# Kernel optimization log

Measured on AMD Instinct MI355X. Metric: run time of the kernel, lower is better.

## Reference

```python
import jax, jax.numpy as jnp
import numpy as np

OH, OW = 32, 32          # adaptive pool output size
NUM_KERNELS = 2
LATENT = 100             # latent_dims = [100, 100]
S = (OH // 2) * (OW // 2)  # in_spatial = 256


def adaptive_avg_pool(x, oh, ow):
    # exact-divisor adaptive avg pool == block mean
    B, C, H, W = x.shape
    return x.reshape(B, C, oh, H // oh, ow, W // ow).mean(axis=(3, 5))


def setup_inputs() -> dict:
    key = jax.random.key(0)
    k1, k2, k3, k4 = jax.random.split(key, 4)
    x = jax.random.normal(k1, (8, 512, 128, 128), dtype=jnp.float32)
    scale = 1.0 / np.sqrt(S)
    psi_w = jax.random.normal(k2, (NUM_KERNELS, S, LATENT), dtype=jnp.float32) * scale  # visible->latent proj
    phi_w = jax.random.normal(k3, (NUM_KERNELS, S, LATENT), dtype=jnp.float32) * scale  # latent->visible proj
    out_w = jax.random.normal(k4, (S, S), dtype=jnp.float32) * scale                    # output linear over spatial feats
    return {"x": x, "psi_w": psi_w, "phi_w": phi_w, "out_w": out_w}


def reference(x, psi_w, phi_w, out_w):
    B, C, H, W = x.shape
    # GAP: adaptive average pool to (OH, OW)
    xg = adaptive_avg_pool(x, OH, OW)                                   # [B,C,32,32]
    # internal 2x2 avg pool (accounts for in_spatial = h/2 * ceil(w/2))
    v = xg.reshape(B, C, OH // 2, 2, OW // 2, 2).mean(axis=(3, 5))
    v = v.reshape(B, C, S)                                              # channel nodes [B,C,S]
    # visible -> latent affinity (softmax over visible/channel nodes)
    A_v2l = jax.nn.softmax(jnp.einsum('bcs,ksd->bkdc', v, psi_w), axis=-1)  # [B,K,d1,C]
    z = jnp.einsum('bkdc,bcs->bkds', A_v2l, v).reshape(B, NUM_KERNELS * LATENT, S)  # [B,Kd1,S]
    # latent -> latent propagation on normalized features
    zn = z / (jnp.linalg.norm(z, axis=-1, keepdims=True) + 1e-6)
    G = jax.nn.softmax(jnp.einsum('bms,bns->bmn', zn, zn), axis=-1)     # [B,Kd1,Kd1]
    zp = jnp.einsum('bmn,bns->bms', G, z).reshape(B, NUM_KERNELS, LATENT, S)
    # latent -> visible affinity (softmax over latent nodes)
    A_l2v = jax.nn.softmax(jnp.einsum('bcs,ksd->bkcd', v, phi_w), axis=-1)  # [B,K,C,d2]
    out = jnp.einsum('bkcd,bkds->bcs', A_l2v, zp)                       # [B,C,S]
    out = jnp.einsum('bcs,st->bct', out, out_w)
    f = v + out                                                          # residual
    attn = jax.nn.sigmoid(f.mean(axis=-1))                               # [B,C]
    return attn[:, :, None, None]                                        # [B,C,1,1]
```

## Files before the change

### kernel.cpp

```cpp
#include <hip/hip_runtime.h>
#include <math.h>

constexpr int Bn = 8, Cn = 512, Sn = 256, Mn = 200, Ln = 100;

constexpr size_t OFF_V    = 0;
constexpr size_t OFF_ZN   = OFF_V    + (size_t)Bn*Cn*Sn;
constexpr size_t OFF_ZNT  = OFF_ZN   + (size_t)Bn*Mn*Sn;
constexpr size_t OFF_P2   = OFF_ZNT  + (size_t)Bn*Sn*Mn;
constexpr size_t OFF_ZW   = OFF_P2   + (size_t)Bn*Cn*Mn;
constexpr size_t OFF_ZPW  = OFF_ZW   + (size_t)Bn*Mn;
constexpr size_t OFF_VSUM = OFF_ZPW  + (size_t)Bn*Mn;
constexpr size_t OFF_WSUM = OFF_VSUM + (size_t)Bn*Cn;

__device__ __forceinline__ float4 blk_max_f4(float4 x, float4* red) {
  #pragma unroll
  for (int o = 32; o; o >>= 1) {
    x.x = fmaxf(x.x, __shfl_xor(x.x, o));
    x.y = fmaxf(x.y, __shfl_xor(x.y, o));
    x.z = fmaxf(x.z, __shfl_xor(x.z, o));
    x.w = fmaxf(x.w, __shfl_xor(x.w, o));
  }
  __syncthreads();
  if ((threadIdx.x & 63) == 0) red[threadIdx.x >> 6] = x;
  __syncthreads();
  float4 r = red[0];
  #pragma unroll
  for (int w = 1; w < 4; ++w) {
    r.x = fmaxf(r.x, red[w].x); r.y = fmaxf(r.y, red[w].y);
    r.z = fmaxf(r.z, red[w].z); r.w = fmaxf(r.w, red[w].w);
  }
  return r;
}
__device__ __forceinline__ float4 blk_sum_f4(float4 x, float4* red) {
  #pragma unroll
  for (int o = 32; o; o >>= 1) {
    x.x += __shfl_xor(x.x, o); x.y += __shfl_xor(x.y, o);
    x.z += __shfl_xor(x.z, o); x.w += __shfl_xor(x.w, o);
  }
  __syncthreads();
  if ((threadIdx.x & 63) == 0) red[threadIdx.x >> 6] = x;
  __syncthreads();
  float4 r = red[0];
  #pragma unroll
  for (int w = 1; w < 4; ++w) {
    r.x += red[w].x; r.y += red[w].y; r.z += red[w].z; r.w += red[w].w;
  }
  return r;
}

__global__ void __launch_bounds__(256) k_pool(const float* __restrict__ x,
                                              const float* __restrict__ ow,
                                              float* __restrict__ ws) {
  int t = threadIdx.x;
  if (blockIdx.x == 4096) {
    const float* row = ow + (size_t)t * Sn;
    float s = 0.f;
    for (int j = 0; j < Sn; j += 4) {
      float4 f = *(const float4*)(row + j);
      s += f.x + f.y + f.z + f.w;
    }
    ws[OFF_WSUM + t] = s;
    return;
  }
  int bc = blockIdx.x;
  const float* plane = x + (size_t)bc * 16384;
  float part[16];
  #pragma unroll
  for (int i = 0; i < 16; ++i) {
    float4 f = *(const float4*)(plane + i * 1024 + t * 4);
    part[i] = f.x + f.y + f.z + f.w;
  }
  __shared__ float lds[256][17];
  #pragma unroll
  for (int i = 0; i < 16; ++i) lds[t][i] = part[i];
  __syncthreads();
  int i = t >> 4, jj = t & 15;
  float s = 0.f;
  #pragma unroll
  for (int r = 0; r < 8; ++r)
    s += lds[32 * r + 2 * jj][i] + lds[32 * r + 2 * jj + 1][i];
  ws[OFF_V + (size_t)bc * 256 + t] = s * (1.0f / 64.0f);
}

struct PszS { float pc[4][256]; float As[4][512]; };
struct P2S  { float vl[8][256]; float t2l[16][104]; };
union MidS { PszS z; P2S p; };

__global__ void __launch_bounds__(256) k_mid(const float* __restrict__ psi,
                                             const float* __restrict__ phi,
                                             float* __restrict__ ws) {
  __shared__ MidS sh;
  __shared__ float4 red4[4];
  int bl = blockIdx.x, t = threadIdx.x;

  if (bl < 400) {
    int b = bl / 50, g = bl % 50, m0 = g * 4;
    const float* v = ws + OFF_V + (size_t)b * Cn * Sn;
    for (int e = t; e < 4 * 256; e += 256) {
      int mm = e >> 8, s = e & 255;
      int m = m0 + mm, k = m / Ln, d = m % Ln;
      sh.z.pc[mm][s] = psi[(size_t)k * Sn * Ln + (size_t)s * Ln + d];
    }
    __syncthreads();
    float acc[2][4];
    #pragma unroll
    for (int mm = 0; mm < 4; ++mm) { acc[0][mm] = 0.f; acc[1][mm] = 0.f; }
    const float* vp0 = v + (size_t)t * Sn;
    const float* vp1 = v + (size_t)(t + 256) * Sn;
    for (int s = 0; s < Sn; s += 4) {
      float4 v0 = *(const float4*)(vp0 + s);
      float4 v1 = *(const float4*)(vp1 + s);
      #pragma unroll
      for (int mm = 0; mm < 4; ++mm) {
        float4 p = *(const float4*)&sh.z.pc[mm][s];
        acc[0][mm] += v0.x * p.x + v0.y * p.y + v0.z * p.z + v0.w * p.w;
        acc[1][mm] += v1.x * p.x + v1.y * p.y + v1.z * p.z + v1.w * p.w;
      }
    }
    float4 a = make_float4(fmaxf(acc[0][0], acc[1][0]), fmaxf(acc[0][1], acc[1][1]),
                           fmaxf(acc[0][2], acc[1][2]), fmaxf(acc[0][3], acc[1][3]));
    float4 mx = blk_max_f4(a, red4);
    float e00 = expf(acc[0][0] - mx.x), e10 = expf(acc[1][0] - mx.x);
    float e01 = expf(acc[0][1] - mx.y), e11 = expf(acc[1][1] - mx.y);
    float e02 = expf(acc[0][2] - mx.z), e12 = expf(acc[1][2] - mx.z);
    float e03 = expf(acc[0][3] - mx.w), e13 = expf(acc[1][3] - mx.w);
    float4 se = blk_sum_f4(make_float4(e00 + e10, e01 + e11, e02 + e12, e03 + e13),
                           red4);
    sh.z.As[0][t] = e00 / se.x; sh.z.As[0][t + 256] = e10 / se.x;
    sh.z.As[1][t] = e01 / se.y; sh.z.As[1][t + 256] = e11 / se.y;
    sh.z.As[2][t] = e02 / se.z; sh.z.As[2][t + 256] = e12 / se.z;
    sh.z.As[3][t] = e03 / se.w; sh.z.As[3][t + 256] = e13 / se.w;
    __syncthreads();
    float zv[4] = {0, 0, 0, 0};
    for (int c = 0; c < Cn; c += 4) {
      float w0 = v[(size_t)(c + 0) * Sn + t];
      float w1 = v[(size_t)(c + 1) * Sn + t];
      float w2 = v[(size_t)(c + 2) * Sn + t];
      float w3 = v[(size_t)(c + 3) * Sn + t];
      #pragma unroll
      for (int mm = 0; mm < 4; ++mm) {
        float4 aa = *(const float4*)&sh.z.As[mm][c];
        zv[mm] += aa.x * w0 + aa.y * w1 + aa.z * w2 + aa.w * w3;
      }
    }
    float wsv = ws[OFF_WSUM + t];
    float4 n2 = blk_sum_f4(make_float4(zv[0]*zv[0], zv[1]*zv[1],
                                       zv[2]*zv[2], zv[3]*zv[3]), red4);
    float4 zw = blk_sum_f4(make_float4(zv[0]*wsv, zv[1]*wsv,
                                       zv[2]*wsv, zv[3]*wsv), red4);
    float zn0 = zv[0] * (1.0f / (sqrtf(n2.x) + 1e-6f));
    float zn1 = zv[1] * (1.0f / (sqrtf(n2.y) + 1e-6f));
    float zn2 = zv[2] * (1.0f / (sqrtf(n2.z) + 1e-6f));
    float zn3 = zv[3] * (1.0f / (sqrtf(n2.w) + 1e-6f));
    float* zo = ws + OFF_ZN + ((size_t)b * Mn + m0) * Sn;
    zo[0 * Sn + t] = zn0; zo[1 * Sn + t] = zn1;
    zo[2 * Sn + t] = zn2; zo[3 * Sn + t] = zn3;
    *(float4*)&ws[OFF_ZNT + ((size_t)b * Sn + t) * Mn + m0] =
        make_float4(zn0, zn1, zn2, zn3);
    if (t == 0) {
      float* zwp = ws + OFF_ZW + (size_t)b * Mn + m0;
      zwp[0] = zw.x; zwp[1] = zw.y; zwp[2] = zw.z; zwp[3] = zw.w;
    }
  } else {
    int bl2 = bl - 400;
    int b = bl2 >> 6, cgrp = bl2 & 63, c0 = cgrp * 8;
    const float* v = ws + OFF_V + ((size_t)b * Cn + c0) * Sn;
    #pragma unroll
    for (int cc = 0; cc < 8; ++cc) sh.p.vl[cc][t] = v[(size_t)cc * Sn + t];
    __syncthreads();
    int k = t >> 7, d = t & 127;
    int dd = d < Ln ? d : Ln - 1;
    const float* pp = phi + (size_t)k * Sn * Ln + dd;
    float acc[8] = {0, 0, 0, 0, 0, 0, 0, 0};
    for (int s = 0; s < Sn; s += 4) {
      float p0 = pp[(size_t)(s + 0) * Ln];
      float p1 = pp[(size_t)(s + 1) * Ln];
      float p2 = pp[(size_t)(s + 2) * Ln];
      float p3 = pp[(size_t)(s + 3) * Ln];
      #pragma unroll
      for (int cc = 0; cc < 8; ++cc) {
        float4 vv = *(const float4*)&sh.p.vl[cc][s];
        acc[cc] += vv.x * p0 + vv.y * p1 + vv.z * p2 + vv.w * p3;
      }
    }
    if (d < Ln) {
      #pragma unroll
      for (int cc = 0; cc < 8; ++cc) sh.p.t2l[k * 8 + cc][d] = acc[cc];
    }
    __syncthreads();
    int gg = t >> 4, l = t & 15;
    int k2 = gg >> 3, cc2 = gg & 7;
    float mx = -1e30f;
    for (int dq = l; dq < Ln; dq += 16) mx = fmaxf(mx, sh.p.t2l[gg][dq]);
    #pragma unroll
    for (int o = 8; o; o >>= 1) mx = fmaxf(mx, __shfl_xor(mx, o));
    float se = 0.f;
    for (int dq = l; dq < Ln; dq += 16) se += expf(sh.p.t2l[gg][dq] - mx);
    #pragma unroll
    for (int o = 8; o; o >>= 1) se += __shfl_xor(se, o);
    float* p2row = ws + OFF_P2 + ((size_t)b * Cn + c0 + cc2) * Mn + k2 * Ln;
    for (int dq = l; dq < Ln; dq += 16)
      p2row[dq] = expf(sh.p.t2l[gg][dq] - mx) / se;
    if (k2 == 0) {
      float vs = 0.f;
      for (int i2 = 0; i2 < 16; ++i2) vs += sh.p.vl[cc2][i2 * 16 + l];
      #pragma unroll
      for (int o = 8; o; o >>= 1) vs += __shfl_xor(vs, o);
      if (l == 0) ws[OFF_VSUM + (size_t)b * Cn + c0 + cc2] = vs;
    }
  }
}

__global__ void __launch_bounds__(256) k_gram(float* __restrict__ ws) {
  int bl = blockIdx.x, t = threadIdx.x;
  int b = bl / 50, g = bl % 50, m0 = g * 4;
  __shared__ __align__(16) float zl[4][256];
  __shared__ float zwl[200];
  __shared__ float4 red4[4];
  const float* zn  = ws + OFF_ZN  + (size_t)b * Mn * Sn;
  const float* znT = ws + OFF_ZNT + (size_t)b * Sn * Mn;
  #pragma unroll
  for (int mm = 0; mm < 4; ++mm)
    zl[mm][t] = zn[(size_t)(m0 + mm) * Sn + t];
  if (t < Mn) zwl[t] = ws[OFF_ZW + (size_t)b * Mn + t];
  __syncthreads();
  bool act = t < Mn;
  float dot[4] = {0, 0, 0, 0};
  if (act) {
    const float* zc = znT + t;
    for (int s = 0; s < Sn; s += 4) {
      float c0v = zc[(size_t)(s + 0) * Mn], c1v = zc[(size_t)(s + 1) * Mn];
      float c2v = zc[(size_t)(s + 2) * Mn], c3v = zc[(size_t)(s + 3) * Mn];
      #pragma unroll
      for (int mm = 0; mm < 4; ++mm) {
        float4 za = *(const float4*)&zl[mm][s];
        dot[mm] += za.x * c0v + za.y * c1v + za.z * c2v + za.w * c3v;
      }
    }
  }
  float4 e;
  e.x = act ? expf(dot[0]) : 0.f;
  e.y = act ? expf(dot[1]) : 0.f;
  e.z = act ? expf(dot[2]) : 0.f;
  e.w = act ? expf(dot[3]) : 0.f;
  float4 se = blk_sum_f4(e, red4);
  float zwn = act ? zwl[t] : 0.f;
  float4 sez = blk_sum_f4(make_float4(e.x*zwn, e.y*zwn, e.z*zwn, e.w*zwn), red4);
  if (t == 0) {
    float* zp = ws + OFF_ZPW + (size_t)b * Mn + m0;
    zp[0] = sez.x / se.x; zp[1] = sez.y / se.y;
    zp[2] = sez.z / se.z; zp[3] = sez.w / se.w;
  }
}

__global__ void __launch_bounds__(256) k_dot(float* __restrict__ ws,
                                             float* __restrict__ out) {
  int bl = blockIdx.x, t = threadIdx.x;
  int b = bl >> 6, cg = bl & 63, c0 = cg * 8;
  __shared__ float zpl[200];
  if (t < Mn) zpl[t] = ws[OFF_ZPW + (size_t)b * Mn + t];
  __syncthreads();
  int c = c0 + (t >> 5), l = t & 31;
  const float* p2 = ws + OFF_P2 + ((size_t)b * Cn + c) * Mn;
  float acc = 0.f;
  for (int m = l; m < Mn; m += 32) acc += p2[m] * zpl[m];
  #pragma unroll
  for (int o = 16; o; o >>= 1) acc += __shfl_xor(acc, o);
  if (l == 0) {
    float f = (ws[OFF_VSUM + (size_t)b * Cn + c] + acc) * (1.0f / 256.0f);
    out[(size_t)b * Cn + c] = 1.0f / (1.0f + expf(-f));
  }
}

extern "C" void kernel_launch(void* const* d_in, const int* in_sizes, int n_in,
                              void* d_out, int out_size, void* d_ws, size_t ws_size,
                              hipStream_t stream) {
  const float* x   = (const float*)d_in[0];
  const float* psi = (const float*)d_in[1];
  const float* phi = (const float*)d_in[2];
  const float* ow  = (const float*)d_in[3];
  float* out = (float*)d_out;
  float* ws  = (float*)d_ws;

  hipLaunchKernelGGL(k_pool, dim3(4097), dim3(256), 0, stream, x, ow, ws);
  hipLaunchKernelGGL(k_mid,  dim3(912),  dim3(256), 0, stream, psi, phi, ws);
  hipLaunchKernelGGL(k_gram, dim3(400),  dim3(256), 0, stream, ws);
  hipLaunchKernelGGL(k_dot,  dim3(512),  dim3(256), 0, stream, ws, out);
}
```

Measured before the change: 136.6 us.

## Double thread count in k_mid and k_gram with split reductions

Raises the block size of k_mid and k_gram from 256 to 512 threads. The channel and spatial reduction loops are split between the two half-blocks, and the partial results are combined through shared memory. The goal is more latency hiding in these small, latency-bound kernels. The cost is extra shared memory, extra barriers and a combine step.

```diff
diff --git a/kernel.cpp b/kernel.cpp
--- a/kernel.cpp
+++ b/kernel.cpp
@@ -12,6 +12,7 @@
 constexpr size_t OFF_VSUM = OFF_ZPW  + (size_t)Bn*Mn;
 constexpr size_t OFF_WSUM = OFF_VSUM + (size_t)Bn*Cn;
 
+template<int NW>
 __device__ __forceinline__ float4 blk_max_f4(float4 x, float4* red) {
   #pragma unroll
   for (int o = 32; o; o >>= 1) {
@@ -25,12 +26,13 @@
   __syncthreads();
   float4 r = red[0];
   #pragma unroll
-  for (int w = 1; w < 4; ++w) {
+  for (int w = 1; w < NW; ++w) {
     r.x = fmaxf(r.x, red[w].x); r.y = fmaxf(r.y, red[w].y);
     r.z = fmaxf(r.z, red[w].z); r.w = fmaxf(r.w, red[w].w);
   }
   return r;
 }
+template<int NW>
 __device__ __forceinline__ float4 blk_sum_f4(float4 x, float4* red) {
   #pragma unroll
   for (int o = 32; o; o >>= 1) {
@@ -42,7 +44,7 @@
   __syncthreads();
   float4 r = red[0];
   #pragma unroll
-  for (int w = 1; w < 4; ++w) {
+  for (int w = 1; w < NW; ++w) {
     r.x += red[w].x; r.y += red[w].y; r.z += red[w].z; r.w += red[w].w;
   }
   return r;
@@ -82,81 +84,89 @@
   ws[OFF_V + (size_t)bc * 256 + t] = s * (1.0f / 64.0f);
 }
 
-struct PszS { float pc[4][256]; float As[4][512]; };
-struct P2S  { float vl[8][256]; float t2l[16][104]; };
+struct PszS { float pc[4][256]; float As[4][512]; float zpart[2][4][256]; };
+struct P2S  { float vl[8][256]; float t2p[2][16][104]; };
 union MidS { PszS z; P2S p; };
 
-__global__ void __launch_bounds__(256) k_mid(const float* __restrict__ psi,
+__global__ void __launch_bounds__(512) k_mid(const float* __restrict__ psi,
                                              const float* __restrict__ phi,
                                              float* __restrict__ ws) {
   __shared__ MidS sh;
-  __shared__ float4 red4[4];
+  __shared__ float4 red4[8];
   int bl = blockIdx.x, t = threadIdx.x;
 
   if (bl < 400) {
     int b = bl / 50, g = bl % 50, m0 = g * 4;
     const float* v = ws + OFF_V + (size_t)b * Cn * Sn;
-    for (int e = t; e < 4 * 256; e += 256) {
+    for (int e = t; e < 4 * 256; e += 512) {
       int mm = e >> 8, s = e & 255;
       int m = m0 + mm, k = m / Ln, d = m % Ln;
       sh.z.pc[mm][s] = psi[(size_t)k * Sn * Ln + (size_t)s * Ln + d];
     }
     __syncthreads();
-    float acc[2][4];
-    #pragma unroll
-    for (int mm = 0; mm < 4; ++mm) { acc[0][mm] = 0.f; acc[1][mm] = 0.f; }
-    const float* vp0 = v + (size_t)t * Sn;
-    const float* vp1 = v + (size_t)(t + 256) * Sn;
+    float acc[4] = {0, 0, 0, 0};
+    const float* vp = v + (size_t)t * Sn;
     for (int s = 0; s < Sn; s += 4) {
-      float4 v0 = *(const float4*)(vp0 + s);
-      float4 v1 = *(const float4*)(vp1 + s);
+      float4 vv = *(const float4*)(vp + s);
       #pragma unroll
       for (int mm = 0; mm < 4; ++mm) {
         float4 p = *(const float4*)&sh.z.pc[mm][s];
-        acc[0][mm] += v0.x * p.x + v0.y * p.y + v0.z * p.z + v0.w * p.w;
-        acc[1][mm] += v1.x * p.x + v1.y * p.y + v1.z * p.z + v1.w * p.w;
-      }
-    }
-    float4 a = make_float4(fmaxf(acc[0][0], acc[1][0]), fmaxf(acc[0][1], acc[1][1]),
-                           fmaxf(acc[0][2], acc[1][2]), fmaxf(acc[0][3], acc[1][3]));
-    float4 mx = blk_max_f4(a, red4);
-    float e00 = expf(acc[0][0] - mx.x), e10 = expf(acc[1][0] - mx.x);
-    float e01 = expf(acc[0][1] - mx.y), e11 = expf(acc[1][1] - mx.y);
-    float e02 = expf(acc[0][2] - mx.z), e12 = expf(acc[1][2] - mx.z);
-    float e03 = expf(acc[0][3] - mx.w), e13 = expf(acc[1][3] - mx.w);
-    float4 se = blk_sum_f4(make_float4(e00 + e10, e01 + e11, e02 + e12, e03 + e13),
-                           red4);
-    sh.z.As[0][t] = e00 / se.x; sh.z.As[0][t + 256] = e10 / se.x;
-    sh.z.As[1][t] = e01 / se.y; sh.z.As[1][t + 256] = e11 / se.y;
-    sh.z.As[2][t] = e02 / se.z; sh.z.As[2][t + 256] = e12 / se.z;
-    sh.z.As[3][t] = e03 / se.w; sh.z.As[3][t + 256] = e13 / se.w;
+        acc[mm] += vv.x * p.x + vv.y * p.y + vv.z * p.z + vv.w * p.w;
+      }
+    }
+    {
+      float4 a = make_float4(acc[0], acc[1], acc[2], acc[3]);
+      float4 mx = blk_max_f4<8>(a, red4);
+      float4 e;
+      e.x = expf(a.x - mx.x); e.y = expf(a.y - mx.y);
+      e.z = expf(a.z - mx.z); e.w = expf(a.w - mx.w);
+      float4 se = blk_sum_f4<8>(e, red4);
+      sh.z.As[0][t] = e.x / se.x;
+      sh.z.As[1][t] = e.y / se.y;
+      sh.z.As[2][t] = e.z / se.z;
+      sh.z.As[3][t] = e.w / se.w;
+    }
+    __syncthreads();
+    int h = t >> 8, s2 = t & 255;
+    float a2[4] = {0, 0, 0, 0};
+    const float* vb = v + (size_t)h * 256 * Sn;
+    for (int c = 0; c < 256; c += 4) {
+      float w0 = vb[(size_t)(c + 0) * Sn + s2];
+      float w1 = vb[(size_t)(c + 1) * Sn + s2];
+      float w2 = vb[(size_t)(c + 2) * Sn + s2];
+      float w3 = vb[(size_t)(c + 3) * Sn + s2];
+      #pragma unroll
+      for (int mm = 0; mm < 4; ++mm) {
+        float4 aa = *(const float4*)&sh.z.As[mm][h * 256 + c];
+        a2[mm] += aa.x * w0 + aa.y * w1 + aa.z * w2 + aa.w * w3;
+      }
+    }
+    #pragma unroll
+    for (int mm = 0; mm < 4; ++mm) sh.z.zpart[h][mm][s2] = a2[mm];
     __syncthreads();
     float zv[4] = {0, 0, 0, 0};
-    for (int c = 0; c < Cn; c += 4) {
-      float w0 = v[(size_t)(c + 0) * Sn + t];
-      float w1 = v[(size_t)(c + 1) * Sn + t];
-      float w2 = v[(size_t)(c + 2) * Sn + t];
-      float w3 = v[(size_t)(c + 3) * Sn + t];
-      #pragma unroll
-      for (int mm = 0; mm < 4; ++mm) {
-        float4 aa = *(const float4*)&sh.z.As[mm][c];
-        zv[mm] += aa.x * w0 + aa.y * w1 + aa.z * w2 + aa.w * w3;
-      }
-    }
-    float wsv = ws[OFF_WSUM + t];
-    float4 n2 = blk_sum_f4(make_float4(zv[0]*zv[0], zv[1]*zv[1],
-                                       zv[2]*zv[2], zv[3]*zv[3]), red4);
-    float4 zw = blk_sum_f4(make_float4(zv[0]*wsv, zv[1]*wsv,
-                                       zv[2]*wsv, zv[3]*wsv), red4);
-    float zn0 = zv[0] * (1.0f / (sqrtf(n2.x) + 1e-6f));
-    float zn1 = zv[1] * (1.0f / (sqrtf(n2.y) + 1e-6f));
-    float zn2 = zv[2] * (1.0f / (sqrtf(n2.z) + 1e-6f));
-    float zn3 = zv[3] * (1.0f / (sqrtf(n2.w) + 1e-6f));
-    float* zo = ws + OFF_ZN + ((size_t)b * Mn + m0) * Sn;
-    zo[0 * Sn + t] = zn0; zo[1 * Sn + t] = zn1;
-    zo[2 * Sn + t] = zn2; zo[3 * Sn + t] = zn3;
-    *(float4*)&ws[OFF_ZNT + ((size_t)b * Sn + t) * Mn + m0] =
-        make_float4(zn0, zn1, zn2, zn3);
+    float wsv = 0.f;
+    if (t < 256) {
+      wsv = ws[OFF_WSUM + t];
+      #pragma unroll
+      for (int mm = 0; mm < 4; ++mm)
+        zv[mm] = sh.z.zpart[0][mm][t] + sh.z.zpart[1][mm][t];
+    }
+    float4 n2 = blk_sum_f4<8>(make_float4(zv[0]*zv[0], zv[1]*zv[1],
+                                          zv[2]*zv[2], zv[3]*zv[3]), red4);
+    float4 zw = blk_sum_f4<8>(make_float4(zv[0]*wsv, zv[1]*wsv,
+                                          zv[2]*wsv, zv[3]*wsv), red4);
+    if (t < 256) {
+      float zn0 = zv[0] * (1.0f / (sqrtf(n2.x) + 1e-6f));
+      float zn1 = zv[1] * (1.0f / (sqrtf(n2.y) + 1e-6f));
+      float zn2 = zv[2] * (1.0f / (sqrtf(n2.z) + 1e-6f));
+      float zn3 = zv[3] * (1.0f / (sqrtf(n2.w) + 1e-6f));
+      float* zo = ws + OFF_ZN + ((size_t)b * Mn + m0) * Sn;
+      zo[0 * Sn + t] = zn0; zo[1 * Sn + t] = zn1;
+      zo[2 * Sn + t] = zn2; zo[3 * Sn + t] = zn3;
+      *(float4*)&ws[OFF_ZNT + ((size_t)b * Sn + t) * Mn + m0] =
+          make_float4(zn0, zn1, zn2, zn3);
+    }
     if (t == 0) {
       float* zwp = ws + OFF_ZW + (size_t)b * Mn + m0;
       zwp[0] = zw.x; zwp[1] = zw.y; zwp[2] = zw.z; zwp[3] = zw.w;
@@ -165,14 +175,19 @@
     int bl2 = bl - 400;
     int b = bl2 >> 6, cgrp = bl2 & 63, c0 = cgrp * 8;
     const float* v = ws + OFF_V + ((size_t)b * Cn + c0) * Sn;
-    #pragma unroll
-    for (int cc = 0; cc < 8; ++cc) sh.p.vl[cc][t] = v[(size_t)cc * Sn + t];
-    __syncthreads();
-    int k = t >> 7, d = t & 127;
+    for (int e = t; e < 8 * 256; e += 512) {
+      int cc = e >> 8, s = e & 255;
+      sh.p.vl[cc][s] = v[(size_t)cc * Sn + s];
+    }
+    __syncthreads();
+    int h = t >> 8, r = t & 255;
+    int k = r >> 7, d = r & 127;
     int dd = d < Ln ? d : Ln - 1;
     const float* pp = phi + (size_t)k * Sn * Ln + dd;
     float acc[8] = {0, 0, 0, 0, 0, 0, 0, 0};
-    for (int s = 0; s < Sn; s += 4) {
+    int sbase = h * 128;
+    for (int si = 0; si < 128; si += 4) {
+      int s = sbase + si;
       float p0 = pp[(size_t)(s + 0) * Ln];
       float p1 = pp[(size_t)(s + 1) * Ln];
       float p2 = pp[(size_t)(s + 2) * Ln];
@@ -185,50 +200,62 @@
     }
     if (d < Ln) {
       #pragma unroll
-      for (int cc = 0; cc < 8; ++cc) sh.p.t2l[k * 8 + cc][d] = acc[cc];
-    }
-    __syncthreads();
-    int gg = t >> 4, l = t & 15;
-    int k2 = gg >> 3, cc2 = gg & 7;
-    float mx = -1e30f;
-    for (int dq = l; dq < Ln; dq += 16) mx = fmaxf(mx, sh.p.t2l[gg][dq]);
-    #pragma unroll
-    for (int o = 8; o; o >>= 1) mx = fmaxf(mx, __shfl_xor(mx, o));
-    float se = 0.f;
-    for (int dq = l; dq < Ln; dq += 16) se += expf(sh.p.t2l[gg][dq] - mx);
-    #pragma unroll
-    for (int o = 8; o; o >>= 1) se += __shfl_xor(se, o);
-    float* p2row = ws + OFF_P2 + ((size_t)b * Cn + c0 + cc2) * Mn + k2 * Ln;
-    for (int dq = l; dq < Ln; dq += 16)
-      p2row[dq] = expf(sh.p.t2l[gg][dq] - mx) / se;
-    if (k2 == 0) {
-      float vs = 0.f;
-      for (int i2 = 0; i2 < 16; ++i2) vs += sh.p.vl[cc2][i2 * 16 + l];
-      #pragma unroll
-      for (int o = 8; o; o >>= 1) vs += __shfl_xor(vs, o);
-      if (l == 0) ws[OFF_VSUM + (size_t)b * Cn + c0 + cc2] = vs;
-    }
-  }
-}
-
-__global__ void __launch_bounds__(256) k_gram(float* __restrict__ ws) {
+      for (int cc = 0; cc < 8; ++cc) sh.p.t2p[h][k * 8 + cc][d] = acc[cc];
+    }
+    __syncthreads();
+    for (int e = t; e < 16 * 104; e += 512) {
+      int row = e / 104, dq = e % 104;
+      if (dq < Ln) sh.p.t2p[0][row][dq] += sh.p.t2p[1][row][dq];
+    }
+    __syncthreads();
+    if (t < 256) {
+      int gg = t >> 4, l = t & 15;
+      int k2 = gg >> 3, cc2 = gg & 7;
+      float mx = -1e30f;
+      for (int dq = l; dq < Ln; dq += 16) mx = fmaxf(mx, sh.p.t2p[0][gg][dq]);
+      #pragma unroll
+      for (int o = 8; o; o >>= 1) mx = fmaxf(mx, __shfl_xor(mx, o));
+      float se = 0.f;
+      for (int dq = l; dq < Ln; dq += 16) se += expf(sh.p.t2p[0][gg][dq] - mx);
+      #pragma unroll
+      for (int o = 8; o; o >>= 1) se += __shfl_xor(se, o);
+      float* p2row = ws + OFF_P2 + ((size_t)b * Cn + c0 + cc2) * Mn + k2 * Ln;
+      for (int dq = l; dq < Ln; dq += 16)
+        p2row[dq] = expf(sh.p.t2p[0][gg][dq] - mx) / se;
+      if (k2 == 0) {
+        float vs = 0.f;
+        for (int i2 = 0; i2 < 16; ++i2) vs += sh.p.vl[cc2][i2 * 16 + l];
+        #pragma unroll
+        for (int o = 8; o; o >>= 1) vs += __shfl_xor(vs, o);
+        if (l == 0) ws[OFF_VSUM + (size_t)b * Cn + c0 + cc2] = vs;
+      }
+    }
+  }
+}
+
+__global__ void __launch_bounds__(512) k_gram(float* __restrict__ ws) {
   int bl = blockIdx.x, t = threadIdx.x;
   int b = bl / 50, g = bl % 50, m0 = g * 4;
   __shared__ __align__(16) float zl[4][256];
   __shared__ float zwl[200];
-  __shared__ float4 red4[4];
+  __shared__ float4 dotp[2][256];
+  __shared__ float4 red4[8];
   const float* zn  = ws + OFF_ZN  + (size_t)b * Mn * Sn;
   const float* znT = ws + OFF_ZNT + (size_t)b * Sn * Mn;
-  #pragma unroll
-  for (int mm = 0; mm < 4; ++mm)
-    zl[mm][t] = zn[(size_t)(m0 + mm) * Sn + t];
+  for (int e = t; e < 4 * 256; e += 512) {
+    int mm = e >> 8, s = e & 255;
+    zl[mm][s] = zn[(size_t)(m0 + mm) * Sn + s];
+  }
   if (t < Mn) zwl[t] = ws[OFF_ZW + (size_t)b * Mn + t];
   __syncthreads();
-  bool act = t < Mn;
+  int h = t >> 8, n = t & 255;
+  bool act = n < Mn;
   float dot[4] = {0, 0, 0, 0};
   if (act) {
-    const float* zc = znT + t;
-    for (int s = 0; s < Sn; s += 4) {
+    const float* zc = znT + n;
+    int sbase = h * 128;
+    for (int si = 0; si < 128; si += 4) {
+      int s = sbase + si;
       float c0v = zc[(size_t)(s + 0) * Mn], c1v = zc[(size_t)(s + 1) * Mn];
       float c2v = zc[(size_t)(s + 2) * Mn], c3v = zc[(size_t)(s + 3) * Mn];
       #pragma unroll
@@ -238,14 +265,18 @@
       }
     }
   }
-  float4 e;
-  e.x = act ? expf(dot[0]) : 0.f;
-  e.y = act ? expf(dot[1]) : 0.f;
-  e.z = act ? expf(dot[2]) : 0.f;
-  e.w = act ? expf(dot[3]) : 0.f;
-  float4 se = blk_sum_f4(e, red4);
-  float zwn = act ? zwl[t] : 0.f;
-  float4 sez = blk_sum_f4(make_float4(e.x*zwn, e.y*zwn, e.z*zwn, e.w*zwn), red4);
+  dotp[h][n] = make_float4(dot[0], dot[1], dot[2], dot[3]);
+  __syncthreads();
+  float4 e = make_float4(0.f, 0.f, 0.f, 0.f);
+  float zwn = 0.f;
+  if (t < 256 && t < Mn) {
+    float4 d0 = dotp[0][t], d1 = dotp[1][t];
+    e.x = expf(d0.x + d1.x); e.y = expf(d0.y + d1.y);
+    e.z = expf(d0.z + d1.z); e.w = expf(d0.w + d1.w);
+    zwn = zwl[t];
+  }
+  float4 se = blk_sum_f4<8>(e, red4);
+  float4 sez = blk_sum_f4<8>(make_float4(e.x*zwn, e.y*zwn, e.z*zwn, e.w*zwn), red4);
   if (t == 0) {
     float* zp = ws + OFF_ZPW + (size_t)b * Mn + m0;
     zp[0] = sez.x / se.x; zp[1] = sez.y / se.y;
@@ -283,7 +314,7 @@
   float* ws  = (float*)d_ws;
 
   hipLaunchKernelGGL(k_pool, dim3(4097), dim3(256), 0, stream, x, ow, ws);
-  hipLaunchKernelGGL(k_mid,  dim3(912),  dim3(256), 0, stream, psi, phi, ws);
-  hipLaunchKernelGGL(k_gram, dim3(400),  dim3(256), 0, stream, ws);
+  hipLaunchKernelGGL(k_mid,  dim3(912),  dim3(512), 0, stream, psi, phi, ws);
+  hipLaunchKernelGGL(k_gram, dim3(400),  dim3(512), 0, stream, ws);
   hipLaunchKernelGGL(k_dot,  dim3(512),  dim3(256), 0, stream, ws, out);
 }
```

New measurement: 142.6 us. +4.4%, slower.

## Fuse gram and output kernels into mid kernel using per-batch atomic counters

Applied to the files above, without the earlier changes.

Merges the gram-softmax and final dot/sigmoid stages into the mid kernel. Per-batch global atomic counters with spin-wait act as cross-block barriers, which removes two launches and the ZN and P2 workspace round-trips. The pool kernel now reads 8x8 blocks directly with float4 loads instead of staging partial sums through LDS, and it also zeroes the counters. Spinning across blocks requires all 912 blocks to be co-resident (launch bounds 256,4 hint at this), otherwise the kernel can deadlock.

```diff
diff --git a/kernel.cpp b/kernel.cpp
--- a/kernel.cpp
+++ b/kernel.cpp
@@ -4,14 +4,13 @@
 constexpr int Bn = 8, Cn = 512, Sn = 256, Mn = 200, Ln = 100;
 
 constexpr size_t OFF_V    = 0;
-constexpr size_t OFF_ZN   = OFF_V    + (size_t)Bn*Cn*Sn;
-constexpr size_t OFF_ZNT  = OFF_ZN   + (size_t)Bn*Mn*Sn;
-constexpr size_t OFF_P2   = OFF_ZNT  + (size_t)Bn*Sn*Mn;
-constexpr size_t OFF_ZW   = OFF_P2   + (size_t)Bn*Cn*Mn;
-constexpr size_t OFF_ZPW  = OFF_ZW   + (size_t)Bn*Mn;
-constexpr size_t OFF_VSUM = OFF_ZPW  + (size_t)Bn*Mn;
-constexpr size_t OFF_WSUM = OFF_VSUM + (size_t)Bn*Cn;
-
+constexpr size_t OFF_ZNT  = OFF_V   + (size_t)Bn*Cn*Sn;
+constexpr size_t OFF_ZW   = OFF_ZNT + (size_t)Bn*Sn*Mn;
+constexpr size_t OFF_ZPW  = OFF_ZW  + (size_t)Bn*Mn;
+constexpr size_t OFF_WSUM = OFF_ZPW + (size_t)Bn*Mn;
+constexpr size_t OFF_CTR  = OFF_WSUM + Sn;
+
+template<int NW>
 __device__ __forceinline__ float4 blk_max_f4(float4 x, float4* red) {
   #pragma unroll
   for (int o = 32; o; o >>= 1) {
@@ -25,12 +24,13 @@
   __syncthreads();
   float4 r = red[0];
   #pragma unroll
-  for (int w = 1; w < 4; ++w) {
+  for (int w = 1; w < NW; ++w) {
     r.x = fmaxf(r.x, red[w].x); r.y = fmaxf(r.y, red[w].y);
     r.z = fmaxf(r.z, red[w].z); r.w = fmaxf(r.w, red[w].w);
   }
   return r;
 }
+template<int NW>
 __device__ __forceinline__ float4 blk_sum_f4(float4 x, float4* red) {
   #pragma unroll
   for (int o = 32; o; o >>= 1) {
@@ -42,7 +42,7 @@
   __syncthreads();
   float4 r = red[0];
   #pragma unroll
-  for (int w = 1; w < 4; ++w) {
+  for (int w = 1; w < NW; ++w) {
     r.x += red[w].x; r.y += red[w].y; r.z += red[w].z; r.w += red[w].w;
   }
   return r;
@@ -53,6 +53,8 @@
                                               float* __restrict__ ws) {
   int t = threadIdx.x;
   if (blockIdx.x == 4096) {
+    unsigned* ctr = (unsigned*)(ws + OFF_CTR);
+    ctr[t] = 0u; ctr[t + 256] = 0u;
     const float* row = ow + (size_t)t * Sn;
     float s = 0.f;
     for (int j = 0; j < Sn; j += 4) {
@@ -63,35 +65,29 @@
     return;
   }
   int bc = blockIdx.x;
-  const float* plane = x + (size_t)bc * 16384;
-  float part[16];
-  #pragma unroll
-  for (int i = 0; i < 16; ++i) {
-    float4 f = *(const float4*)(plane + i * 1024 + t * 4);
-    part[i] = f.x + f.y + f.z + f.w;
-  }
-  __shared__ float lds[256][17];
-  #pragma unroll
-  for (int i = 0; i < 16; ++i) lds[t][i] = part[i];
-  __syncthreads();
   int i = t >> 4, jj = t & 15;
+  const float* base = x + (size_t)bc * 16384 + (size_t)(i * 8) * 128 + jj * 8;
   float s = 0.f;
   #pragma unroll
-  for (int r = 0; r < 8; ++r)
-    s += lds[32 * r + 2 * jj][i] + lds[32 * r + 2 * jj + 1][i];
+  for (int r = 0; r < 8; ++r) {
+    float4 a = *(const float4*)(base + r * 128);
+    float4 b = *(const float4*)(base + r * 128 + 4);
+    s += a.x + a.y + a.z + a.w + b.x + b.y + b.z + b.w;
+  }
   ws[OFF_V + (size_t)bc * 256 + t] = s * (1.0f / 64.0f);
 }
 
-struct PszS { float pc[4][256]; float As[4][512]; };
-struct P2S  { float vl[8][256]; float t2l[16][104]; };
+struct PszS { float pczl[4][256]; float As[4][512]; float zwl[200]; };
+struct P2S  { float vl[8][256]; float t2l[16][104]; float zpl[200]; float vsl[8]; };
 union MidS { PszS z; P2S p; };
 
-__global__ void __launch_bounds__(256) k_mid(const float* __restrict__ psi,
-                                             const float* __restrict__ phi,
-                                             float* __restrict__ ws) {
+__global__ void __launch_bounds__(256, 4)
+k_mid(const float* __restrict__ psi, const float* __restrict__ phi,
+      float* __restrict__ out, float* __restrict__ ws) {
   __shared__ MidS sh;
   __shared__ float4 red4[4];
   int bl = blockIdx.x, t = threadIdx.x;
+  unsigned* ctr = (unsigned*)(ws + OFF_CTR);
 
   if (bl < 400) {
     int b = bl / 50, g = bl % 50, m0 = g * 4;
@@ -99,7 +95,7 @@
     for (int e = t; e < 4 * 256; e += 256) {
       int mm = e >> 8, s = e & 255;
       int m = m0 + mm, k = m / Ln, d = m % Ln;
-      sh.z.pc[mm][s] = psi[(size_t)k * Sn * Ln + (size_t)s * Ln + d];
+      sh.z.pczl[mm][s] = psi[(size_t)k * Sn * Ln + (size_t)s * Ln + d];
     }
     __syncthreads();
     float acc[2][4];
@@ -112,20 +108,20 @@
       float4 v1 = *(const float4*)(vp1 + s);
       #pragma unroll
       for (int mm = 0; mm < 4; ++mm) {
-        float4 p = *(const float4*)&sh.z.pc[mm][s];
+        float4 p = *(const float4*)&sh.z.pczl[mm][s];
         acc[0][mm] += v0.x * p.x + v0.y * p.y + v0.z * p.z + v0.w * p.w;
         acc[1][mm] += v1.x * p.x + v1.y * p.y + v1.z * p.z + v1.w * p.w;
       }
     }
     float4 a = make_float4(fmaxf(acc[0][0], acc[1][0]), fmaxf(acc[0][1], acc[1][1]),
                            fmaxf(acc[0][2], acc[1][2]), fmaxf(acc[0][3], acc[1][3]));
-    float4 mx = blk_max_f4(a, red4);
+    float4 mx = blk_max_f4<4>(a, red4);
     float e00 = expf(acc[0][0] - mx.x), e10 = expf(acc[1][0] - mx.x);
     float e01 = expf(acc[0][1] - mx.y), e11 = expf(acc[1][1] - mx.y);
     float e02 = expf(acc[0][2] - mx.z), e12 = expf(acc[1][2] - mx.z);
     float e03 = expf(acc[0][3] - mx.w), e13 = expf(acc[1][3] - mx.w);
-    float4 se = blk_sum_f4(make_float4(e00 + e10, e01 + e11, e02 + e12, e03 + e13),
-                           red4);
+    float4 se = blk_sum_f4<4>(make_float4(e00 + e10, e01 + e11, e02 + e12, e03 + e13),
+                              red4);
     sh.z.As[0][t] = e00 / se.x; sh.z.As[0][t + 256] = e10 / se.x;
     sh.z.As[1][t] = e01 / se.y; sh.z.As[1][t + 256] = e11 / se.y;
     sh.z.As[2][t] = e02 / se.z; sh.z.As[2][t + 256] = e12 / se.z;
@@ -144,29 +140,67 @@
       }
     }
     float wsv = ws[OFF_WSUM + t];
-    float4 n2 = blk_sum_f4(make_float4(zv[0]*zv[0], zv[1]*zv[1],
-                                       zv[2]*zv[2], zv[3]*zv[3]), red4);
-    float4 zw = blk_sum_f4(make_float4(zv[0]*wsv, zv[1]*wsv,
-                                       zv[2]*wsv, zv[3]*wsv), red4);
+    float4 n2 = blk_sum_f4<4>(make_float4(zv[0]*zv[0], zv[1]*zv[1],
+                                          zv[2]*zv[2], zv[3]*zv[3]), red4);
+    float4 zw = blk_sum_f4<4>(make_float4(zv[0]*wsv, zv[1]*wsv,
+                                          zv[2]*wsv, zv[3]*wsv), red4);
     float zn0 = zv[0] * (1.0f / (sqrtf(n2.x) + 1e-6f));
     float zn1 = zv[1] * (1.0f / (sqrtf(n2.y) + 1e-6f));
     float zn2 = zv[2] * (1.0f / (sqrtf(n2.z) + 1e-6f));
     float zn3 = zv[3] * (1.0f / (sqrtf(n2.w) + 1e-6f));
-    float* zo = ws + OFF_ZN + ((size_t)b * Mn + m0) * Sn;
-    zo[0 * Sn + t] = zn0; zo[1 * Sn + t] = zn1;
-    zo[2 * Sn + t] = zn2; zo[3 * Sn + t] = zn3;
+    sh.z.pczl[0][t] = zn0; sh.z.pczl[1][t] = zn1;
+    sh.z.pczl[2][t] = zn2; sh.z.pczl[3][t] = zn3;
     *(float4*)&ws[OFF_ZNT + ((size_t)b * Sn + t) * Mn + m0] =
         make_float4(zn0, zn1, zn2, zn3);
     if (t == 0) {
       float* zwp = ws + OFF_ZW + (size_t)b * Mn + m0;
       zwp[0] = zw.x; zwp[1] = zw.y; zwp[2] = zw.z; zwp[3] = zw.w;
     }
+    __threadfence();
+    if (t == 0) atomicAdd(&ctr[b * 32], 1u);
+    while (__hip_atomic_load(&ctr[b * 32], __ATOMIC_RELAXED,
+                             __HIP_MEMORY_SCOPE_AGENT) < 50u)
+      __builtin_amdgcn_s_sleep(16);
+    __threadfence();
+    for (int e = t; e < Mn; e += 256) sh.z.zwl[e] = ws[OFF_ZW + (size_t)b * Mn + e];
+    __syncthreads();
+    bool act = t < Mn;
+    float dot[4] = {0, 0, 0, 0};
+    if (act) {
+      const float* zc = ws + OFF_ZNT + (size_t)b * Sn * Mn + t;
+      for (int s = 0; s < Sn; s += 4) {
+        float c0v = zc[(size_t)(s + 0) * Mn], c1v = zc[(size_t)(s + 1) * Mn];
+        float c2v = zc[(size_t)(s + 2) * Mn], c3v = zc[(size_t)(s + 3) * Mn];
+        #pragma unroll
+        for (int mm = 0; mm < 4; ++mm) {
+          float4 za = *(const float4*)&sh.z.pczl[mm][s];
+          dot[mm] += za.x * c0v + za.y * c1v + za.z * c2v + za.w * c3v;
+        }
+      }
+    }
+    float4 e;
+    e.x = act ? expf(dot[0]) : 0.f;
+    e.y = act ? expf(dot[1]) : 0.f;
+    e.z = act ? expf(dot[2]) : 0.f;
+    e.w = act ? expf(dot[3]) : 0.f;
+    float4 seg = blk_sum_f4<4>(e, red4);
+    float zwn = act ? sh.z.zwl[t] : 0.f;
+    float4 sez = blk_sum_f4<4>(make_float4(e.x*zwn, e.y*zwn, e.z*zwn, e.w*zwn), red4);
+    if (t == 0) {
+      float* zp = ws + OFF_ZPW + (size_t)b * Mn + m0;
+      zp[0] = sez.x / seg.x; zp[1] = sez.y / seg.y;
+      zp[2] = sez.z / seg.z; zp[3] = sez.w / seg.w;
+    }
+    __threadfence();
+    if (t == 0) atomicAdd(&ctr[256 + b * 32], 1u);
   } else {
     int bl2 = bl - 400;
     int b = bl2 >> 6, cgrp = bl2 & 63, c0 = cgrp * 8;
     const float* v = ws + OFF_V + ((size_t)b * Cn + c0) * Sn;
-    #pragma unroll
-    for (int cc = 0; cc < 8; ++cc) sh.p.vl[cc][t] = v[(size_t)cc * Sn + t];
+    for (int e = t; e < 8 * 256; e += 256) {
+      int cc = e >> 8, s = e & 255;
+      sh.p.vl[cc][s] = v[(size_t)cc * Sn + s];
+    }
     __syncthreads();
     int k = t >> 7, d = t & 127;
     int dd = d < Ln ? d : Ln - 1;
@@ -190,85 +224,40 @@
     __syncthreads();
     int gg = t >> 4, l = t & 15;
     int k2 = gg >> 3, cc2 = gg & 7;
-    float mx = -1e30f;
-    for (int dq = l; dq < Ln; dq += 16) mx = fmaxf(mx, sh.p.t2l[gg][dq]);
-    #pragma unroll
-    for (int o = 8; o; o >>= 1) mx = fmaxf(mx, __shfl_xor(mx, o));
-    float se = 0.f;
-    for (int dq = l; dq < Ln; dq += 16) se += expf(sh.p.t2l[gg][dq] - mx);
-    #pragma unroll
-    for (int o = 8; o; o >>= 1) se += __shfl_xor(se, o);
-    float* p2row = ws + OFF_P2 + ((size_t)b * Cn + c0 + cc2) * Mn + k2 * Ln;
+    float mxr = -1e30f;
+    for (int dq = l; dq < Ln; dq += 16) mxr = fmaxf(mxr, sh.p.t2l[gg][dq]);
+    #pragma unroll
+    for (int o = 8; o; o >>= 1) mxr = fmaxf(mxr, __shfl_xor(mxr, o));
+    float ser = 0.f;
+    for (int dq = l; dq < Ln; dq += 16) ser += expf(sh.p.t2l[gg][dq] - mxr);
+    #pragma unroll
+    for (int o = 8; o; o >>= 1) ser += __shfl_xor(ser, o);
     for (int dq = l; dq < Ln; dq += 16)
-      p2row[dq] = expf(sh.p.t2l[gg][dq] - mx) / se;
+      sh.p.t2l[gg][dq] = expf(sh.p.t2l[gg][dq] - mxr) / ser;
     if (k2 == 0) {
       float vs = 0.f;
       for (int i2 = 0; i2 < 16; ++i2) vs += sh.p.vl[cc2][i2 * 16 + l];
       #pragma unroll
       for (int o = 8; o; o >>= 1) vs += __shfl_xor(vs, o);
-      if (l == 0) ws[OFF_VSUM + (size_t)b * Cn + c0 + cc2] = vs;
-    }
-  }
-}
-
-__global__ void __launch_bounds__(256) k_gram(float* __restrict__ ws) {
-  int bl = blockIdx.x, t = threadIdx.x;
-  int b = bl / 50, g = bl % 50, m0 = g * 4;
-  __shared__ __align__(16) float zl[4][256];
-  __shared__ float zwl[200];
-  __shared__ float4 red4[4];
-  const float* zn  = ws + OFF_ZN  + (size_t)b * Mn * Sn;
-  const float* znT = ws + OFF_ZNT + (size_t)b * Sn * Mn;
-  #pragma unroll
-  for (int mm = 0; mm < 4; ++mm)
-    zl[mm][t] = zn[(size_t)(m0 + mm) * Sn + t];
-  if (t < Mn) zwl[t] = ws[OFF_ZW + (size_t)b * Mn + t];
-  __syncthreads();
-  bool act = t < Mn;
-  float dot[4] = {0, 0, 0, 0};
-  if (act) {
-    const float* zc = znT + t;
-    for (int s = 0; s < Sn; s += 4) {
-      float c0v = zc[(size_t)(s + 0) * Mn], c1v = zc[(size_t)(s + 1) * Mn];
-      float c2v = zc[(size_t)(s + 2) * Mn], c3v = zc[(size_t)(s + 3) * Mn];
-      #pragma unroll
-      for (int mm = 0; mm < 4; ++mm) {
-        float4 za = *(const float4*)&zl[mm][s];
-        dot[mm] += za.x * c0v + za.y * c1v + za.z * c2v + za.w * c3v;
-      }
-    }
-  }
-  float4 e;
-  e.x = act ? expf(dot[0]) : 0.f;
-  e.y = act ? expf(dot[1]) : 0.f;
-  e.z = act ? expf(dot[2]) : 0.f;
-  e.w = act ? expf(dot[3]) : 0.f;
-  float4 se = blk_sum_f4(e, red4);
-  float zwn = act ? zwl[t] : 0.f;
-  float4 sez = blk_sum_f4(make_float4(e.x*zwn, e.y*zwn, e.z*zwn, e.w*zwn), red4);
-  if (t == 0) {
-    float* zp = ws + OFF_ZPW + (size_t)b * Mn + m0;
-    zp[0] = sez.x / se.x; zp[1] = sez.y / se.y;
-    zp[2] = sez.z / se.z; zp[3] = sez.w / se.w;
-  }
-}
-
-__global__ void __launch_bounds__(256) k_dot(float* __restrict__ ws,
-                                             float* __restrict__ out) {
-  int bl = blockIdx.x, t = threadIdx.x;
-  int b = bl >> 6, cg = bl & 63, c0 = cg * 8;
-  __shared__ float zpl[200];
-  if (t < Mn) zpl[t] = ws[OFF_ZPW + (size_t)b * Mn + t];
-  __syncthreads();
-  int c = c0 + (t >> 5), l = t & 31;
-  const float* p2 = ws + OFF_P2 + ((size_t)b * Cn + c) * Mn;
-  float acc = 0.f;
-  for (int m = l; m < Mn; m += 32) acc += p2[m] * zpl[m];
-  #pragma unroll
-  for (int o = 16; o; o >>= 1) acc += __shfl_xor(acc, o);
-  if (l == 0) {
-    float f = (ws[OFF_VSUM + (size_t)b * Cn + c] + acc) * (1.0f / 256.0f);
-    out[(size_t)b * Cn + c] = 1.0f / (1.0f + expf(-f));
+      if (l == 0) sh.p.vsl[cc2] = vs;
+    }
+    __syncthreads();
+    while (__hip_atomic_load(&ctr[256 + b * 32], __ATOMIC_RELAXED,
+                             __HIP_MEMORY_SCOPE_AGENT) < 50u)
+      __builtin_amdgcn_s_sleep(16);
+    __threadfence();
+    for (int e = t; e < Mn; e += 256) sh.p.zpl[e] = ws[OFF_ZPW + (size_t)b * Mn + e];
+    __syncthreads();
+    int cc = t >> 5, l2 = t & 31;
+    float accd = 0.f;
+    for (int m = l2; m < Mn; m += 32)
+      accd += sh.p.t2l[(m >= Ln ? 8 : 0) + cc][m >= Ln ? m - Ln : m] * sh.p.zpl[m];
+    #pragma unroll
+    for (int o = 16; o; o >>= 1) accd += __shfl_xor(accd, o);
+    if (l2 == 0) {
+      float f = (sh.p.vsl[cc] + accd) * (1.0f / 256.0f);
+      out[(size_t)b * Cn + c0 + cc] = 1.0f / (1.0f + expf(-f));
+    }
   }
 }
 
@@ -283,7 +272,5 @@
   float* ws  = (float*)d_ws;
 
   hipLaunchKernelGGL(k_pool, dim3(4097), dim3(256), 0, stream, x, ow, ws);
-  hipLaunchKernelGGL(k_mid,  dim3(912),  dim3(256), 0, stream, psi, phi, ws);
-  hipLaunchKernelGGL(k_gram, dim3(400),  dim3(256), 0, stream, ws);
-  hipLaunchKernelGGL(k_dot,  dim3(512),  dim3(256), 0, stream, ws, out);
-}
+  hipLaunchKernelGGL(k_mid,  dim3(912),  dim3(256), 0, stream, psi, phi, out, ws);
+}
```

Result: slower. 294.2 us (+115.4%).
